# Kernel optimization log

Measured on AMD Instinct MI355X. Metric: run time of the kernel, lower is better.

## Reference

```python
import jax, jax.numpy as jnp
import numpy as np

B, N, M = 8, 4096, 4096


def setup_inputs() -> dict:
    key = jax.random.key(0)
    ks = jax.random.split(key, 8)
    return {
        "x_aligned": jax.random.normal(ks[0], (B, N, 3), dtype=jnp.float32),
        "y": jax.random.normal(ks[1], (B, M, 3), dtype=jnp.float32),
        "R": jax.random.normal(ks[2], (B, 3, 3), dtype=jnp.float32),
        "S": jax.random.normal(ks[3], (B, 3), dtype=jnp.float32),
        "t": jax.random.normal(ks[4], (B, 3, 1), dtype=jnp.float32),
        "R_gt": jax.random.normal(ks[5], (B, 3, 3), dtype=jnp.float32),
        "S_gt": jax.random.normal(ks[6], (B, 3), dtype=jnp.float32),
        "t_gt": jax.random.normal(ks[7], (B, 3), dtype=jnp.float32),
    }


def chamfer_distance(x, y):
    # x: [B,N,3], y: [B,M,3]; bidirectional mean squared NN distance
    xn = jnp.sum(x * x, axis=-1)                      # [B,N]
    yn = jnp.sum(y * y, axis=-1)                      # [B,M]
    xy = jnp.einsum('bnd,bmd->bnm', x, y)             # [B,N,M]
    d2 = xn[:, :, None] + yn[:, None, :] - 2.0 * xy   # [B,N,M] squared dists
    cham_x = jnp.mean(jnp.min(d2, axis=2), axis=1)    # [B] x -> y
    cham_y = jnp.mean(jnp.min(d2, axis=1), axis=1)    # [B] y -> x
    return jnp.mean(cham_x) + jnp.mean(cham_y)        # batch mean, summed dirs


def reference(x_aligned, y, R, S, t, R_gt, S_gt, t_gt):
    t = jnp.squeeze(t)                                # [B,3]
    eye = jnp.eye(3, dtype=R.dtype)
    R_loss = jnp.einsum('bij,bkj->bik', R, R_gt) - eye  # R @ R_gt^T - I
    L_reg = (jnp.sum(R_loss * R_loss)
             + jnp.sum((S - S_gt) ** 2)
             + jnp.sum((t - t_gt) ** 2))
    L_chamfer = chamfer_distance(x_aligned, y)
    return L_reg + L_chamfer
```

## Files before the change

kernel.cpp:

```cpp
#include <hip/hip_runtime.h>

#define BB 8
#define NN 4096
#define MC 128
#define NCHUNK (NN / MC)
#define KPT 16
#define TPB 128
#define PTS_PER_BLOCK (TPB * KPT)
#define NPTS (2 * BB * NN)


typedef __attribute__((ext_vector_type(2))) float f2;

__device__ __forceinline__ f2 pk_fma(f2 a, f2 b, f2 c) {
  f2 d;
  asm("v_pk_fma_f32 %0, %1, %2, %3" : "=v"(d) : "v"(a), "v"(b), "v"(c));
  return d;
}

__global__ __launch_bounds__(TPB) void chamfer_partial(
    const float* __restrict__ X, const float* __restrict__ Y,
    float* __restrict__ partial, float* __restrict__ out) {
  __shared__ float4 lxy[MC / 2];
  __shared__ float4 lzw[MC / 2];
  const int tid = threadIdx.x;
  const int zb  = blockIdx.z;
  const int b   = zb & (BB - 1);
  const int dir = zb >> 3;
  const float* pts  = dir ? (Y + b * NN * 3) : (X + b * NN * 3);
  const float* refs = dir ? (X + b * NN * 3) : (Y + b * NN * 3);
  const int c = blockIdx.y;

  if (blockIdx.x == 0 && blockIdx.y == 0 && blockIdx.z == 0 && tid == 0)
    out[0] = 0.0f;

  if (tid < MC / 2) {
    const int j = c * MC + 2 * tid;
    const float a0 = refs[j * 3 + 0], a1 = refs[j * 3 + 1], a2 = refs[j * 3 + 2];
    const float b0 = refs[j * 3 + 3], b1 = refs[j * 3 + 4], b2 = refs[j * 3 + 5];
    lxy[tid] = make_float4(-2.0f * a0, -2.0f * b0, -2.0f * a1, -2.0f * b1);
    lzw[tid] = make_float4(-2.0f * a2, -2.0f * b2,
                           a0 * a0 + a1 * a1 + a2 * a2,
                           b0 * b0 + b1 * b1 + b2 * b2);
  }

  f2 px2[KPT], py2[KPT], pz2[KPT];
  float m[KPT];
  const int p0 = blockIdx.x * PTS_PER_BLOCK + tid;
#pragma unroll
  for (int k = 0; k < KPT; k++) {
    const int p = p0 + k * TPB;
    const float qx = pts[p * 3 + 0];
    const float qy = pts[p * 3 + 1];
    const float qz = pts[p * 3 + 2];
    px2[k] = (f2){qx, qx};
    py2[k] = (f2){qy, qy};
    pz2[k] = (f2){qz, qz};
    m[k] = 1e30f;
  }
  __syncthreads();

#pragma unroll 2
  for (int jp = 0; jp < MC / 2; jp++) {
    const float4 wxy = lxy[jp];
    const float4 wzw = lzw[jp];
    const f2 xp = (f2){wxy.x, wxy.y};
    const f2 yp = (f2){wxy.z, wxy.w};
    const f2 zp = (f2){wzw.x, wzw.y};
    const f2 wp = (f2){wzw.z, wzw.w};
#pragma unroll
    for (int k = 0; k < KPT; k++) {
      f2 s = pk_fma(pz2[k], zp, wp);
      s = pk_fma(py2[k], yp, s);
      s = pk_fma(px2[k], xp, s);
      m[k] = fminf(m[k], fminf(s.x, s.y));
    }
  }

#pragma unroll
  for (int k = 0; k < KPT; k++) {
    const int p = p0 + k * TPB;
    const float qx = px2[k].x, qy = py2[k].x, qz = pz2[k].x;
    const float pn = qx * qx + qy * qy + qz * qz;
    partial[(c * (2 * BB) + zb) * NN + p] = m[k] + pn;
  }
}

__global__ __launch_bounds__(256) void chamfer_reduce(
    const float* __restrict__ partial,
    const float* __restrict__ R, const float* __restrict__ S,
    const float* __restrict__ t, const float* __restrict__ Rgt,
    const float* __restrict__ Sgt, const float* __restrict__ tgt,
    float* __restrict__ out) {
  const int tid = threadIdx.x;
  const int q0 = blockIdx.x * 1024 + tid;
  float s = 0.0f;
#pragma unroll
  for (int kk = 0; kk < 4; kk++) {
    const int q = q0 + kk * 256;
    float m = 1e30f;
#pragma unroll
    for (int c = 0; c < NCHUNK; c++)
      m = fminf(m, partial[c * NPTS + q]);
    s += m;
  }
  for (int o = 32; o > 0; o >>= 1) s += __shfl_down(s, o);
  __shared__ float wsum[4];
  if ((tid & 63) == 0) wsum[tid >> 6] = s;
  __syncthreads();
  if (tid == 0) {
    const float bs = wsum[0] + wsum[1] + wsum[2] + wsum[3];
    atomicAdd(out, bs * (1.0f / (float)(BB * NN)));
  }

  if (blockIdx.x == 0) {
    float v = 0.0f;
    if (tid < 72) {
      const int b = tid / 9, ik = tid % 9, i = ik / 3, k = ik % 3;
      const float* Rb = R + b * 9;
      const float* Gb = Rgt + b * 9;
      float d = Rb[i * 3 + 0] * Gb[k * 3 + 0] +
                Rb[i * 3 + 1] * Gb[k * 3 + 1] +
                Rb[i * 3 + 2] * Gb[k * 3 + 2];
      d -= (i == k) ? 1.0f : 0.0f;
      v = d * d;
    } else if (tid < 96) {
      const int i = tid - 72;
      const float d = S[i] - Sgt[i];
      v = d * d;
    } else if (tid < 120) {
      const int i = tid - 96;
      const float d = t[i] - tgt[i];
      v = d * d;
    }
    for (int o = 32; o > 0; o >>= 1) v += __shfl_down(v, o);
    __shared__ float rsum[4];
    if ((tid & 63) == 0) rsum[tid >> 6] = v;
    __syncthreads();
    if (tid == 0) atomicAdd(out, rsum[0] + rsum[1] + rsum[2] + rsum[3]);
  }
}

extern "C" void kernel_launch(void* const* d_in, const int* in_sizes, int n_in,
                              void* d_out, int out_size, void* d_ws, size_t ws_size,
                              hipStream_t stream) {
  const float* X   = (const float*)d_in[0];
  const float* Y   = (const float*)d_in[1];
  const float* R   = (const float*)d_in[2];
  const float* S   = (const float*)d_in[3];
  const float* t   = (const float*)d_in[4];
  const float* Rgt = (const float*)d_in[5];
  const float* Sgt = (const float*)d_in[6];
  const float* tgt = (const float*)d_in[7];

  float* partial = (float*)d_ws;
  float* out     = (float*)d_out;

  dim3 gA(NN / PTS_PER_BLOCK, NCHUNK, 2 * BB);
  chamfer_partial<<<gA, TPB, 0, stream>>>(X, Y, partial, out);

  chamfer_reduce<<<NPTS / 1024, 256, 0, stream>>>(partial, R, S, t, Rgt, Sgt, tgt, out);
}
```

Baseline: 101.1 us.

## Replace partial-min buffer with atomicMin on clamped float bits, halve chunk size

Instead of writing every chunk's partial minimum to a large workspace and scanning all chunks in the reduce kernel, each block now clamps its distance to be non-negative and folds it into a per-point minimum with an integer atomicMin on the float bit pattern. The buffer is initialised by a memset, and the reduce kernel becomes a plain vectorised sum. The reference chunk size is halved, which doubles the grid and the atomic traffic in exchange for more parallelism. Clamping to zero changes results slightly when the expanded-form distance goes negative, and the extra memset adds a launch.

```diff
diff --git a/kernel.cpp b/kernel.cpp
--- a/kernel.cpp
+++ b/kernel.cpp
@@ -2,7 +2,7 @@
 
 #define BB 8
 #define NN 4096
-#define MC 128
+#define MC 64
 #define NCHUNK (NN / MC)
 #define KPT 16
 #define TPB 128
@@ -20,7 +20,7 @@
 
 __global__ __launch_bounds__(TPB) void chamfer_partial(
     const float* __restrict__ X, const float* __restrict__ Y,
-    float* __restrict__ partial, float* __restrict__ out) {
+    unsigned int* __restrict__ nnmin, float* __restrict__ out) {
   __shared__ float4 lxy[MC / 2];
   __shared__ float4 lzw[MC / 2];
   const int tid = threadIdx.x;
@@ -82,28 +82,23 @@
     const int p = p0 + k * TPB;
     const float qx = px2[k].x, qy = py2[k].x, qz = pz2[k].x;
     const float pn = qx * qx + qy * qy + qz * qz;
-    partial[(c * (2 * BB) + zb) * NN + p] = m[k] + pn;
+    const float d2 = fmaxf(m[k] + pn, 0.0f);
+    atomicMin(&nnmin[zb * NN + p], __float_as_uint(d2));
   }
 }
 
 __global__ __launch_bounds__(256) void chamfer_reduce(
-    const float* __restrict__ partial,
+    const float* __restrict__ nnmin,
     const float* __restrict__ R, const float* __restrict__ S,
     const float* __restrict__ t, const float* __restrict__ Rgt,
     const float* __restrict__ Sgt, const float* __restrict__ tgt,
     float* __restrict__ out) {
   const int tid = threadIdx.x;
-  const int q0 = blockIdx.x * 1024 + tid;
-  float s = 0.0f;
-#pragma unroll
-  for (int kk = 0; kk < 4; kk++) {
-    const int q = q0 + kk * 256;
-    float m = 1e30f;
-#pragma unroll
-    for (int c = 0; c < NCHUNK; c++)
-      m = fminf(m, partial[c * NPTS + q]);
-    s += m;
-  }
+  const int base = blockIdx.x * 2048;
+  const float4* v = (const float4*)nnmin;
+  const float4 a0 = v[(base >> 2) + tid];
+  const float4 a1 = v[(base >> 2) + 256 + tid];
+  float s = (a0.x + a0.y) + (a0.z + a0.w) + (a1.x + a1.y) + (a1.z + a1.w);
   for (int o = 32; o > 0; o >>= 1) s += __shfl_down(s, o);
   __shared__ float wsum[4];
   if ((tid & 63) == 0) wsum[tid >> 6] = s;
@@ -114,7 +109,7 @@
   }
 
   if (blockIdx.x == 0) {
-    float v = 0.0f;
+    float v2 = 0.0f;
     if (tid < 72) {
       const int b = tid / 9, ik = tid % 9, i = ik / 3, k = ik % 3;
       const float* Rb = R + b * 9;
@@ -123,19 +118,19 @@
                 Rb[i * 3 + 1] * Gb[k * 3 + 1] +
                 Rb[i * 3 + 2] * Gb[k * 3 + 2];
       d -= (i == k) ? 1.0f : 0.0f;
-      v = d * d;
+      v2 = d * d;
     } else if (tid < 96) {
       const int i = tid - 72;
       const float d = S[i] - Sgt[i];
-      v = d * d;
+      v2 = d * d;
     } else if (tid < 120) {
       const int i = tid - 96;
       const float d = t[i] - tgt[i];
-      v = d * d;
+      v2 = d * d;
     }
-    for (int o = 32; o > 0; o >>= 1) v += __shfl_down(v, o);
+    for (int o = 32; o > 0; o >>= 1) v2 += __shfl_down(v2, o);
     __shared__ float rsum[4];
-    if ((tid & 63) == 0) rsum[tid >> 6] = v;
+    if ((tid & 63) == 0) rsum[tid >> 6] = v2;
     __syncthreads();
     if (tid == 0) atomicAdd(out, rsum[0] + rsum[1] + rsum[2] + rsum[3]);
   }
@@ -153,11 +148,14 @@
   const float* Sgt = (const float*)d_in[6];
   const float* tgt = (const float*)d_in[7];
 
-  float* partial = (float*)d_ws;
-  float* out     = (float*)d_out;
+  unsigned int* nnmin = (unsigned int*)d_ws;
+  float* out = (float*)d_out;
+
+  hipMemsetAsync(nnmin, 0x7F, NPTS * sizeof(unsigned int), stream);
 
   dim3 gA(NN / PTS_PER_BLOCK, NCHUNK, 2 * BB);
-  chamfer_partial<<<gA, TPB, 0, stream>>>(X, Y, partial, out);
+  chamfer_partial<<<gA, TPB, 0, stream>>>(X, Y, nnmin, out);
 
-  chamfer_reduce<<<NPTS / 1024, 256, 0, stream>>>(partial, R, S, t, Rgt, Sgt, tgt, out);
+  chamfer_reduce<<<NPTS / 2048, 256, 0, stream>>>((const float*)nnmin,
+                                                  R, S, t, Rgt, Sgt, tgt, out);
 }
```

New measurement: 99.15 us. No clear change (-1.9%).
